# Kernel tuning notes

Measured on AMD Instinct MI355X. Metric: run time of the kernel, lower is better.

Reference implementation:

```python
import jax, jax.numpy as jnp
from jax import lax
import numpy as np

T, B, X, Y = 24, 16, 32, 32
FS, FM, FC = 64, 16, 16
I = FS + FM + FC  # GRU input size = 96
H = 32            # hidden_size


def setup_inputs() -> dict:
    key = jax.random.key(0)
    ks = jax.random.split(key, 8)
    s = 1.0 / np.sqrt(H)  # pytorch GRU init scale
    return {
        "spatial": jax.random.normal(ks[0], (B, X, Y, FS), jnp.float32),
        "meteorology": jax.random.normal(ks[1], (T, B, X, Y, FM), jnp.float32),
        "context": jax.random.normal(ks[2], (T, B, X, Y, FC), jnp.float32),
        "W_ih": jax.random.uniform(ks[3], (3 * H, I), jnp.float32, -s, s),
        "W_hh": jax.random.uniform(ks[4], (3 * H, H), jnp.float32, -s, s),
        "b_ih": jax.random.uniform(ks[5], (3 * H,), jnp.float32, -s, s),
        "b_hh": jax.random.uniform(ks[6], (3 * H,), jnp.float32, -s, s),
        "W": jax.random.normal(ks[7], (H, FS), jnp.float32),
    }


def _gru_final_state(x, W_ih, W_hh, b_ih, b_hh):
    # x: (T, N, I); returns final hidden state (N, H). PyTorch GRU cell math.
    n_batch = x.shape[1]
    h0 = jnp.zeros((n_batch, H), x.dtype)

    def step(h, xt):
        gi = xt @ W_ih.T + b_ih          # (N, 3H)
        gh = h @ W_hh.T + b_hh           # (N, 3H)
        i_r, i_z, i_n = jnp.split(gi, 3, axis=-1)
        h_r, h_z, h_n = jnp.split(gh, 3, axis=-1)
        r = jax.nn.sigmoid(i_r + h_r)
        z = jax.nn.sigmoid(i_z + h_z)
        n = jnp.tanh(i_n + r * h_n)
        h_new = (1.0 - z) * n + z * h
        return h_new, None

    hT, _ = lax.scan(step, h0, x)
    return hT


def reference(spatial, meteorology, context, W_ih, W_hh, b_ih, b_hh, W):
    # Broadcast static spatial features over time and concat along feature dim.
    t = meteorology.shape[0]
    sp = jnp.broadcast_to(spatial[None], (t,) + spatial.shape)
    x = jnp.concatenate([sp, meteorology, context], axis=-1)  # (T,B,X,Y,I)
    # Batch all spatial positions into one recurrence: (T, B*X*Y, I)
    x = x.reshape(t, B * X * Y, I)
    hT = _gru_final_state(x, W_ih, W_hh, b_ih, b_hh)          # (B*X*Y, H)
    out = hT @ W                                              # (B*X*Y, FS)
    return out.reshape(B, X, Y, FS)
```

## Files before the change

kernel.cpp:

```cpp
#include <hip/hip_runtime.h>
#include <hip/hip_fp16.h>
#include <math.h>


typedef __attribute__((ext_vector_type(8))) short short8;
typedef __attribute__((ext_vector_type(8))) _Float16 half8;
typedef __attribute__((ext_vector_type(4))) float f32x4;
typedef __attribute__((ext_vector_type(4))) unsigned int uix4;

#define NSEQ 16384
#define TSTEPS 24
#define LOG2E 1.44269504088896340736f

__device__ __forceinline__ float exp2_fast(float x) {
#if __has_builtin(__builtin_amdgcn_exp2f)
  return __builtin_amdgcn_exp2f(x);
#else
  return __expf(x * 0.6931471805599453f);
#endif
}

__device__ __forceinline__ unsigned int pk_f16(float a, float b) {
#if __has_builtin(__builtin_amdgcn_cvt_pkrtz)
  auto r = __builtin_amdgcn_cvt_pkrtz(a, b);
  return __builtin_bit_cast(unsigned int, r);
#else
  return (unsigned)__half_as_ushort(__float2half(a)) |
         ((unsigned)__half_as_ushort(__float2half(b)) << 16);
#endif
}

__device__ __forceinline__ unsigned int pk_f16_rn(float a, float b) {
  return (unsigned)__half_as_ushort(__float2half(a)) |
         ((unsigned)__half_as_ushort(__float2half(b)) << 16);
}

__device__ __forceinline__ half8 mk_h8(unsigned int a, unsigned int b,
                                       unsigned int c, unsigned int d) {
  uix4 v = {a, b, c, d};
  return __builtin_bit_cast(half8, v);
}

__device__ __forceinline__ f32x4 mfma_h(half8 a, half8 b, f32x4 c) {
  return __builtin_amdgcn_mfma_f32_16x16x32_f16(a, b, c, 0, 0, 0);
}

__device__ __forceinline__ void barrier_lds() {
  asm volatile("s_waitcnt lgkmcnt(0)" ::: "memory");
  __builtin_amdgcn_s_barrier();
}

__global__ __launch_bounds__(256, 4)
void gru8(const float* __restrict__ spatial,
          const float* __restrict__ met,
          const float* __restrict__ ctx,
          const float* __restrict__ W_ih,
          const float* __restrict__ W_hh,
          const float* __restrict__ b_ih,
          const float* __restrict__ b_hh,
          const float* __restrict__ Wp,
          float* __restrict__ out) {
  __shared__ float xls[2][6][16][20];
  __shared__ unsigned int hbuf[2][2][64][2];

  const int tid = threadIdx.x;
  const int lane = tid & 63;
  const int wv = tid >> 6;
  const int l15 = lane & 15;
  const int c = lane >> 4;
  const int seq = blockIdx.x * 16 + l15;
  const f32x4 zero4 = {0.f, 0.f, 0.f, 0.f};

  ((unsigned int*)hbuf[1])[tid] = 0u;

  if (wv >= 2) {
    const int q = wv - 2;
    half8 wmc[3];
    f32x4 acc_i[3];
#pragma unroll
    for (int g = 0; g < 3; ++g) {
      const float sc = (g < 2) ? LOG2E : (2.0f * LOG2E);
      const int rowb = g * 32 + q * 16;
      const float* wrow = W_ih + (size_t)(rowb + l15) * 96 + 64 + c * 8;
      float4 wa = *(const float4*)wrow;
      float4 wb = *(const float4*)(wrow + 4);
      wmc[g] = mk_h8(pk_f16_rn(wa.x * sc, wa.y * sc),
                     pk_f16_rn(wa.z * sc, wa.w * sc),
                     pk_f16_rn(wb.x * sc, wb.y * sc),
                     pk_f16_rn(wb.z * sc, wb.w * sc));
      float4 vih = *(const float4*)(b_ih + rowb + 4 * c);
      if (g < 2) {
        float4 vhh = *(const float4*)(b_hh + rowb + 4 * c);
        acc_i[g][0] = (vih.x + vhh.x) * sc; acc_i[g][1] = (vih.y + vhh.y) * sc;
        acc_i[g][2] = (vih.z + vhh.z) * sc; acc_i[g][3] = (vih.w + vhh.w) * sc;
      } else {
        acc_i[g][0] = vih.x * sc; acc_i[g][1] = vih.y * sc;
        acc_i[g][2] = vih.z * sc; acc_i[g][3] = vih.w * sc;
      }
    }
#pragma unroll
    for (int kt = 0; kt < 2; ++kt) {
      const float* sp = spatial + (size_t)seq * 64 + kt * 32 + c * 8;
      float4 a0 = *(const float4*)sp;
      float4 a1 = *(const float4*)(sp + 4);
      half8 sf = mk_h8(pk_f16(a0.x, a0.y), pk_f16(a0.z, a0.w),
                       pk_f16(a1.x, a1.y), pk_f16(a1.z, a1.w));
#pragma unroll
      for (int g = 0; g < 3; ++g) {
        const float sc = (g < 2) ? LOG2E : (2.0f * LOG2E);
        const float* wrow = W_ih + (size_t)(g * 32 + q * 16 + l15) * 96 +
                            kt * 32 + c * 8;
        float4 wa = *(const float4*)wrow;
        float4 wb = *(const float4*)(wrow + 4);
        half8 wsp = mk_h8(pk_f16_rn(wa.x * sc, wa.y * sc),
                          pk_f16_rn(wa.z * sc, wa.w * sc),
                          pk_f16_rn(wb.x * sc, wb.y * sc),
                          pk_f16_rn(wb.z * sc, wb.w * sc));
        acc_i[g] = mfma_h(wsp, sf, acc_i[g]);
      }
    }
    const float* lptr = ((c < 2) ? met : ctx) + (size_t)seq * 16 + (c & 1) * 8;
    {
      float4 a0 = *(const float4*)lptr;
      float4 a1 = *(const float4*)(lptr + 4);
      half8 xf = mk_h8(pk_f16(a0.x, a0.y), pk_f16(a0.z, a0.w),
                       pk_f16(a1.x, a1.y), pk_f16(a1.z, a1.w));
#pragma unroll
      for (int g = 0; g < 3; ++g) {
        f32x4 D = mfma_h(wmc[g], xf, acc_i[g]);
        *(f32x4*)&xls[0][g * 2 + q][l15][c * 4] = D;
      }
    }
    float4 xs0a = *(const float4*)(lptr + (size_t)1 * NSEQ * 16);
    float4 xs0b = *(const float4*)(lptr + (size_t)1 * NSEQ * 16 + 4);
    float4 xs1a = *(const float4*)(lptr + (size_t)2 * NSEQ * 16);
    float4 xs1b = *(const float4*)(lptr + (size_t)2 * NSEQ * 16 + 4);

    barrier_lds();

#pragma unroll 2
    for (int t = 0; t < TSTEPS; ++t) {
      float4 xa = (t & 1) ? xs1a : xs0a;
      float4 xb = (t & 1) ? xs1b : xs0b;
      half8 xf = mk_h8(pk_f16(xa.x, xa.y), pk_f16(xa.z, xa.w),
                       pk_f16(xb.x, xb.y), pk_f16(xb.z, xb.w));
      {
        int tf = (t + 3 < TSTEPS) ? (t + 3) : (TSTEPS - 1);
        float4 na = *(const float4*)(lptr + (size_t)tf * NSEQ * 16);
        float4 nb = *(const float4*)(lptr + (size_t)tf * NSEQ * 16 + 4);
        if (t & 1) { xs1a = na; xs1b = nb; } else { xs0a = na; xs0b = nb; }
      }
      const int buf = (t + 1) & 1;
#pragma unroll
      for (int g = 0; g < 3; ++g) {
        f32x4 D = mfma_h(wmc[g], xf, acc_i[g]);
        *(f32x4*)&xls[buf][g * 2 + q][l15][c * 4] = D;
      }
      barrier_lds();
    }
  } else {
    const int p = wv;
    __builtin_amdgcn_s_setprio(1);
    half8 whh[3];
#pragma unroll
    for (int g = 0; g < 3; ++g) {
      const float sc = (g < 2) ? LOG2E : (2.0f * LOG2E);
      const float* wrow = W_hh + (size_t)(g * 32 + p * 16 + l15) * 32;
      float4 a = *(const float4*)(wrow + 4 * c);
      float4 b = *(const float4*)(wrow + 16 + 4 * c);
      whh[g] = mk_h8(pk_f16_rn(a.x * sc, a.y * sc),
                     pk_f16_rn(a.z * sc, a.w * sc),
                     pk_f16_rn(b.x * sc, b.y * sc),
                     pk_f16_rn(b.z * sc, b.w * sc));
    }
    f32x4 bhn4;
    {
      float4 v = *(const float4*)(b_hh + 64 + p * 16 + 4 * c);
      bhn4[0] = 2.0f * LOG2E * v.x; bhn4[1] = 2.0f * LOG2E * v.y;
      bhn4[2] = 2.0f * LOG2E * v.z; bhn4[3] = 2.0f * LOG2E * v.w;
    }
    float hst[4] = {0.f, 0.f, 0.f, 0.f};
    unsigned int own0 = 0u, own1 = 0u;

    barrier_lds();

#pragma unroll 2
    for (int t = 0; t < TSTEPS; ++t) {
      const unsigned int* hp = &hbuf[(t + 1) & 1][1 - p][lane][0];
      unsigned int phx = hp[0], phy = hp[1];
      f32x4 xr = *(const f32x4*)&xls[t & 1][p][l15][c * 4];
      f32x4 xz = *(const f32x4*)&xls[t & 1][2 + p][l15][c * 4];
      f32x4 ti = *(const f32x4*)&xls[t & 1][4 + p][l15][c * 4];

      half8 fh = p ? mk_h8(phx, phy, own0, own1)
                   : mk_h8(own0, own1, phx, phy);

      f32x4 d0 = mfma_h(whh[0], fh, xr);
      f32x4 d1 = mfma_h(whh[1], fh, xz);
      f32x4 dn = mfma_h(whh[2], fh, bhn4);

      float hv_[4];
#pragma unroll
      for (int qq = 0; qq < 4; ++qq) {
        float R = exp2_fast(-d0[qq]);
        float r = __builtin_amdgcn_rcpf(1.0f + R);
        float E = fminf(exp2_fast(-d1[qq]), 1e30f);
        float Y = fmaf(r, dn[qq], ti[qq]);
        float e = fminf(exp2_fast(-Y), 1e30f);
        float oe = 1.0f + e, oE = 1.0f + E;
        float inv = __builtin_amdgcn_rcpf(oE * oe);
        float num = fmaf(hst[qq], oe, fmaf(-E, e, E));
        float hv = num * inv;
        hst[qq] = hv;
        hv_[qq] = hv;
      }
      own0 = pk_f16(hv_[0], hv_[1]);
      own1 = pk_f16(hv_[2], hv_[3]);
      hbuf[t & 1][p][lane][0] = own0;
      hbuf[t & 1][p][lane][1] = own1;

      barrier_lds();
    }

    half8 fh;
    {
      const unsigned int* hp = &hbuf[1][1 - p][lane][0];
      unsigned int phx = hp[0], phy = hp[1];
      fh = p ? mk_h8(phx, phy, own0, own1)
             : mk_h8(own0, own1, phx, phy);
    }
#pragma unroll
    for (int pt = 0; pt < 2; ++pt) {
      int ftile = pt * 2 + p;
      int frow = ftile * 16 + l15;
      const float* wpb = Wp + frow;
      float v[8];
#pragma unroll
      for (int e = 0; e < 8; ++e) {
        int col = (e < 4) ? (4 * c + e) : (16 + 4 * c + (e - 4));
        v[e] = wpb[(size_t)col * 64];
      }
      unsigned int uh[4], ul[4];
#pragma unroll
      for (int e2 = 0; e2 < 4; ++e2) {
        float va = v[2 * e2], vb = v[2 * e2 + 1];
        __half ha = __float2half(va), hb = __float2half(vb);
        float la = va - __half2float(ha), lb = vb - __half2float(hb);
        uh[e2] = (unsigned)__half_as_ushort(ha) |
                 ((unsigned)__half_as_ushort(hb) << 16);
        ul[e2] = pk_f16_rn(la, lb);
      }
      half8 wph = mk_h8(uh[0], uh[1], uh[2], uh[3]);
      half8 wpl = mk_h8(ul[0], ul[1], ul[2], ul[3]);
      f32x4 o = mfma_h(wph, fh, zero4);
      o = mfma_h(wpl, fh, o);
      float* op = out + (size_t)seq * 64 + ftile * 16 + 4 * c;
      *(float4*)op = make_float4(o[0], o[1], o[2], o[3]);
    }
    __builtin_amdgcn_s_setprio(0);
  }
}

extern "C" void kernel_launch(void* const* d_in, const int* in_sizes, int n_in,
                              void* d_out, int out_size, void* d_ws, size_t ws_size,
                              hipStream_t stream) {
  const float* spatial = (const float*)d_in[0];
  const float* met     = (const float*)d_in[1];
  const float* ctx     = (const float*)d_in[2];
  const float* W_ih    = (const float*)d_in[3];
  const float* W_hh    = (const float*)d_in[4];
  const float* b_ih    = (const float*)d_in[5];
  const float* b_hh    = (const float*)d_in[6];
  const float* Wp      = (const float*)d_in[7];
  float* out = (float*)d_out;

  hipLaunchKernelGGL(gru8, dim3(1024), dim3(256), 0, stream,
                     spatial, met, ctx, W_ih, W_hh, b_ih, b_hh, Wp, out);
}
```

Before: 25.16 us.

## Collapse GRU block to single wavefront, removing per-step barriers and LDS handoff

Replaces the 4-wave producer/consumer block with a single 64-thread wave per 16 sequences. That wave preloads all timesteps of meteorology and context into LDS as fp16, computes all 6 gate tiles itself, and keeps the hidden state in registers. This removes per-timestep barriers and the LDS exchange of hidden halves between waves, and software-pipelines the input projection one step ahead. The cost is fewer waves per block and a longer serial chain per wave with more MFMA work. It also relies on occupancy from many small blocks to hide latency.

```diff
diff --git a/kernel.cpp b/kernel.cpp
--- a/kernel.cpp
+++ b/kernel.cpp
@@ -3,7 +3,6 @@
 #include <math.h>
 
 
-typedef __attribute__((ext_vector_type(8))) short short8;
 typedef __attribute__((ext_vector_type(8))) _Float16 half8;
 typedef __attribute__((ext_vector_type(4))) float f32x4;
 typedef __attribute__((ext_vector_type(4))) unsigned int uix4;
@@ -29,29 +28,21 @@
          ((unsigned)__half_as_ushort(__float2half(b)) << 16);
 #endif
 }
-
 __device__ __forceinline__ unsigned int pk_f16_rn(float a, float b) {
   return (unsigned)__half_as_ushort(__float2half(a)) |
          ((unsigned)__half_as_ushort(__float2half(b)) << 16);
 }
-
 __device__ __forceinline__ half8 mk_h8(unsigned int a, unsigned int b,
                                        unsigned int c, unsigned int d) {
   uix4 v = {a, b, c, d};
   return __builtin_bit_cast(half8, v);
 }
-
 __device__ __forceinline__ f32x4 mfma_h(half8 a, half8 b, f32x4 c) {
   return __builtin_amdgcn_mfma_f32_16x16x32_f16(a, b, c, 0, 0, 0);
 }
 
-__device__ __forceinline__ void barrier_lds() {
-  asm volatile("s_waitcnt lgkmcnt(0)" ::: "memory");
-  __builtin_amdgcn_s_barrier();
-}
-
-__global__ __launch_bounds__(256, 4)
-void gru8(const float* __restrict__ spatial,
+__global__ __launch_bounds__(64, 1)
+void gru9(const float* __restrict__ spatial,
           const float* __restrict__ met,
           const float* __restrict__ ctx,
           const float* __restrict__ W_ih,
@@ -60,204 +51,180 @@
           const float* __restrict__ b_hh,
           const float* __restrict__ Wp,
           float* __restrict__ out) {
-  __shared__ float xls[2][6][16][20];
-  __shared__ unsigned int hbuf[2][2][64][2];
-
-  const int tid = threadIdx.x;
-  const int lane = tid & 63;
-  const int wv = tid >> 6;
+  __shared__ unsigned int xst[TSTEPS][16][16];
+
+  const int lane = threadIdx.x & 63;
   const int l15 = lane & 15;
   const int c = lane >> 4;
   const int seq = blockIdx.x * 16 + l15;
   const f32x4 zero4 = {0.f, 0.f, 0.f, 0.f};
 
-  ((unsigned int*)hbuf[1])[tid] = 0u;
-
-  if (wv >= 2) {
-    const int q = wv - 2;
-    half8 wmc[3];
-    f32x4 acc_i[3];
-#pragma unroll
-    for (int g = 0; g < 3; ++g) {
-      const float sc = (g < 2) ? LOG2E : (2.0f * LOG2E);
-      const int rowb = g * 32 + q * 16;
-      const float* wrow = W_ih + (size_t)(rowb + l15) * 96 + 64 + c * 8;
-      float4 wa = *(const float4*)wrow;
-      float4 wb = *(const float4*)(wrow + 4);
-      wmc[g] = mk_h8(pk_f16_rn(wa.x * sc, wa.y * sc),
-                     pk_f16_rn(wa.z * sc, wa.w * sc),
-                     pk_f16_rn(wb.x * sc, wb.y * sc),
-                     pk_f16_rn(wb.z * sc, wb.w * sc));
-      float4 vih = *(const float4*)(b_ih + rowb + 4 * c);
-      if (g < 2) {
-        float4 vhh = *(const float4*)(b_hh + rowb + 4 * c);
-        acc_i[g][0] = (vih.x + vhh.x) * sc; acc_i[g][1] = (vih.y + vhh.y) * sc;
-        acc_i[g][2] = (vih.z + vhh.z) * sc; acc_i[g][3] = (vih.w + vhh.w) * sc;
-      } else {
-        acc_i[g][0] = vih.x * sc; acc_i[g][1] = vih.y * sc;
-        acc_i[g][2] = vih.z * sc; acc_i[g][3] = vih.w * sc;
-      }
-    }
-#pragma unroll
-    for (int kt = 0; kt < 2; ++kt) {
-      const float* sp = spatial + (size_t)seq * 64 + kt * 32 + c * 8;
-      float4 a0 = *(const float4*)sp;
-      float4 a1 = *(const float4*)(sp + 4);
-      half8 sf = mk_h8(pk_f16(a0.x, a0.y), pk_f16(a0.z, a0.w),
-                       pk_f16(a1.x, a1.y), pk_f16(a1.z, a1.w));
-#pragma unroll
-      for (int g = 0; g < 3; ++g) {
-        const float sc = (g < 2) ? LOG2E : (2.0f * LOG2E);
-        const float* wrow = W_ih + (size_t)(g * 32 + q * 16 + l15) * 96 +
-                            kt * 32 + c * 8;
-        float4 wa = *(const float4*)wrow;
-        float4 wb = *(const float4*)(wrow + 4);
-        half8 wsp = mk_h8(pk_f16_rn(wa.x * sc, wa.y * sc),
-                          pk_f16_rn(wa.z * sc, wa.w * sc),
-                          pk_f16_rn(wb.x * sc, wb.y * sc),
-                          pk_f16_rn(wb.z * sc, wb.w * sc));
-        acc_i[g] = mfma_h(wsp, sf, acc_i[g]);
-      }
-    }
-    const float* lptr = ((c < 2) ? met : ctx) + (size_t)seq * 16 + (c & 1) * 8;
-    {
-      float4 a0 = *(const float4*)lptr;
-      float4 a1 = *(const float4*)(lptr + 4);
-      half8 xf = mk_h8(pk_f16(a0.x, a0.y), pk_f16(a0.z, a0.w),
-                       pk_f16(a1.x, a1.y), pk_f16(a1.z, a1.w));
-#pragma unroll
-      for (int g = 0; g < 3; ++g) {
-        f32x4 D = mfma_h(wmc[g], xf, acc_i[g]);
-        *(f32x4*)&xls[0][g * 2 + q][l15][c * 4] = D;
-      }
-    }
-    float4 xs0a = *(const float4*)(lptr + (size_t)1 * NSEQ * 16);
-    float4 xs0b = *(const float4*)(lptr + (size_t)1 * NSEQ * 16 + 4);
-    float4 xs1a = *(const float4*)(lptr + (size_t)2 * NSEQ * 16);
-    float4 xs1b = *(const float4*)(lptr + (size_t)2 * NSEQ * 16 + 4);
-
-    barrier_lds();
-
-#pragma unroll 2
-    for (int t = 0; t < TSTEPS; ++t) {
-      float4 xa = (t & 1) ? xs1a : xs0a;
-      float4 xb = (t & 1) ? xs1b : xs0b;
-      half8 xf = mk_h8(pk_f16(xa.x, xa.y), pk_f16(xa.z, xa.w),
-                       pk_f16(xb.x, xb.y), pk_f16(xb.z, xb.w));
-      {
-        int tf = (t + 3 < TSTEPS) ? (t + 3) : (TSTEPS - 1);
-        float4 na = *(const float4*)(lptr + (size_t)tf * NSEQ * 16);
-        float4 nb = *(const float4*)(lptr + (size_t)tf * NSEQ * 16 + 4);
-        if (t & 1) { xs1a = na; xs1b = nb; } else { xs0a = na; xs0b = nb; }
-      }
-      const int buf = (t + 1) & 1;
-#pragma unroll
-      for (int g = 0; g < 3; ++g) {
-        f32x4 D = mfma_h(wmc[g], xf, acc_i[g]);
-        *(f32x4*)&xls[buf][g * 2 + q][l15][c * 4] = D;
-      }
-      barrier_lds();
-    }
-  } else {
-    const int p = wv;
-    __builtin_amdgcn_s_setprio(1);
-    half8 whh[3];
-#pragma unroll
-    for (int g = 0; g < 3; ++g) {
-      const float sc = (g < 2) ? LOG2E : (2.0f * LOG2E);
-      const float* wrow = W_hh + (size_t)(g * 32 + p * 16 + l15) * 32;
-      float4 a = *(const float4*)(wrow + 4 * c);
-      float4 b = *(const float4*)(wrow + 16 + 4 * c);
-      whh[g] = mk_h8(pk_f16_rn(a.x * sc, a.y * sc),
-                     pk_f16_rn(a.z * sc, a.w * sc),
-                     pk_f16_rn(b.x * sc, b.y * sc),
-                     pk_f16_rn(b.z * sc, b.w * sc));
-    }
-    f32x4 bhn4;
-    {
-      float4 v = *(const float4*)(b_hh + 64 + p * 16 + 4 * c);
-      bhn4[0] = 2.0f * LOG2E * v.x; bhn4[1] = 2.0f * LOG2E * v.y;
-      bhn4[2] = 2.0f * LOG2E * v.z; bhn4[3] = 2.0f * LOG2E * v.w;
-    }
-    float hst[4] = {0.f, 0.f, 0.f, 0.f};
-    unsigned int own0 = 0u, own1 = 0u;
-
-    barrier_lds();
-
-#pragma unroll 2
-    for (int t = 0; t < TSTEPS; ++t) {
-      const unsigned int* hp = &hbuf[(t + 1) & 1][1 - p][lane][0];
-      unsigned int phx = hp[0], phy = hp[1];
-      f32x4 xr = *(const f32x4*)&xls[t & 1][p][l15][c * 4];
-      f32x4 xz = *(const f32x4*)&xls[t & 1][2 + p][l15][c * 4];
-      f32x4 ti = *(const f32x4*)&xls[t & 1][4 + p][l15][c * 4];
-
-      half8 fh = p ? mk_h8(phx, phy, own0, own1)
-                   : mk_h8(own0, own1, phx, phy);
-
-      f32x4 d0 = mfma_h(whh[0], fh, xr);
-      f32x4 d1 = mfma_h(whh[1], fh, xz);
-      f32x4 dn = mfma_h(whh[2], fh, bhn4);
-
-      float hv_[4];
-#pragma unroll
-      for (int qq = 0; qq < 4; ++qq) {
-        float R = exp2_fast(-d0[qq]);
+#pragma unroll
+  for (int tt = 0; tt < 6; ++tt) {
+    const int t = c + tt * 4;
+    const float* mp = met + ((size_t)t * NSEQ + seq) * 16;
+    const float* cp = ctx + ((size_t)t * NSEQ + seq) * 16;
+    float4 m0 = *(const float4*)mp;       float4 m1 = *(const float4*)(mp + 4);
+    float4 m2 = *(const float4*)(mp + 8); float4 m3 = *(const float4*)(mp + 12);
+    float4 c0 = *(const float4*)cp;       float4 c1 = *(const float4*)(cp + 4);
+    float4 c2 = *(const float4*)(cp + 8); float4 c3 = *(const float4*)(cp + 12);
+    unsigned int* dst = &xst[t][l15][0];
+    uix4 w0 = {pk_f16(m0.x, m0.y), pk_f16(m0.z, m0.w),
+               pk_f16(m1.x, m1.y), pk_f16(m1.z, m1.w)};
+    uix4 w1 = {pk_f16(m2.x, m2.y), pk_f16(m2.z, m2.w),
+               pk_f16(m3.x, m3.y), pk_f16(m3.z, m3.w)};
+    uix4 w2 = {pk_f16(c0.x, c0.y), pk_f16(c0.z, c0.w),
+               pk_f16(c1.x, c1.y), pk_f16(c1.z, c1.w)};
+    uix4 w3 = {pk_f16(c2.x, c2.y), pk_f16(c2.z, c2.w),
+               pk_f16(c3.x, c3.y), pk_f16(c3.z, c3.w)};
+    *(uix4*)&dst[0]  = w0;  *(uix4*)&dst[4]  = w1;
+    *(uix4*)&dst[8]  = w2;  *(uix4*)&dst[12] = w3;
+  }
+
+  half8 whh[6], wmc[6];
+  f32x4 acc_i[6], bhnA, bhnB;
+#pragma unroll
+  for (int j = 0; j < 6; ++j) {
+    const float sc = (j < 4) ? LOG2E : (2.0f * LOG2E);
+    const float* wr = W_hh + (size_t)(j * 16 + l15) * 32;
+    float4 a = *(const float4*)(wr + 4 * c);
+    float4 b = *(const float4*)(wr + 16 + 4 * c);
+    whh[j] = mk_h8(pk_f16_rn(a.x * sc, a.y * sc), pk_f16_rn(a.z * sc, a.w * sc),
+                   pk_f16_rn(b.x * sc, b.y * sc), pk_f16_rn(b.z * sc, b.w * sc));
+    const float* mr = W_ih + (size_t)(j * 16 + l15) * 96 + 64 + c * 8;
+    float4 wa = *(const float4*)mr;
+    float4 wb = *(const float4*)(mr + 4);
+    wmc[j] = mk_h8(pk_f16_rn(wa.x * sc, wa.y * sc), pk_f16_rn(wa.z * sc, wa.w * sc),
+                   pk_f16_rn(wb.x * sc, wb.y * sc), pk_f16_rn(wb.z * sc, wb.w * sc));
+    const int rowb = j * 16 + 4 * c;
+    float4 vih = *(const float4*)(b_ih + rowb);
+    if (j < 4) {
+      float4 vhh = *(const float4*)(b_hh + rowb);
+      acc_i[j][0] = (vih.x + vhh.x) * sc; acc_i[j][1] = (vih.y + vhh.y) * sc;
+      acc_i[j][2] = (vih.z + vhh.z) * sc; acc_i[j][3] = (vih.w + vhh.w) * sc;
+    } else {
+      acc_i[j][0] = vih.x * sc; acc_i[j][1] = vih.y * sc;
+      acc_i[j][2] = vih.z * sc; acc_i[j][3] = vih.w * sc;
+    }
+  }
+  {
+    float4 va = *(const float4*)(b_hh + 64 + 4 * c);
+    float4 vb = *(const float4*)(b_hh + 64 + 16 + 4 * c);
+    bhnA[0] = 2.0f * LOG2E * va.x; bhnA[1] = 2.0f * LOG2E * va.y;
+    bhnA[2] = 2.0f * LOG2E * va.z; bhnA[3] = 2.0f * LOG2E * va.w;
+    bhnB[0] = 2.0f * LOG2E * vb.x; bhnB[1] = 2.0f * LOG2E * vb.y;
+    bhnB[2] = 2.0f * LOG2E * vb.z; bhnB[3] = 2.0f * LOG2E * vb.w;
+  }
+
+#pragma unroll
+  for (int kt = 0; kt < 2; ++kt) {
+    const float* sp = spatial + (size_t)seq * 64 + kt * 32 + c * 8;
+    float4 a0 = *(const float4*)sp;
+    float4 a1 = *(const float4*)(sp + 4);
+    half8 sf = mk_h8(pk_f16(a0.x, a0.y), pk_f16(a0.z, a0.w),
+                     pk_f16(a1.x, a1.y), pk_f16(a1.z, a1.w));
+#pragma unroll
+    for (int j = 0; j < 6; ++j) {
+      const float sc = (j < 4) ? LOG2E : (2.0f * LOG2E);
+      const float* wr = W_ih + (size_t)(j * 16 + l15) * 96 + kt * 32 + c * 8;
+      float4 wa = *(const float4*)wr;
+      float4 wb = *(const float4*)(wr + 4);
+      half8 wsp = mk_h8(pk_f16_rn(wa.x * sc, wa.y * sc),
+                        pk_f16_rn(wa.z * sc, wa.w * sc),
+                        pk_f16_rn(wb.x * sc, wb.y * sc),
+                        pk_f16_rn(wb.z * sc, wb.w * sc));
+      acc_i[j] = mfma_h(wsp, sf, acc_i[j]);
+    }
+  }
+
+  f32x4 xacc[6];
+  {
+    uix4 v = *(const uix4*)&xst[0][l15][c * 4];
+    half8 xf = __builtin_bit_cast(half8, v);
+#pragma unroll
+    for (int j = 0; j < 6; ++j) xacc[j] = mfma_h(wmc[j], xf, acc_i[j]);
+  }
+  half8 xf1;
+  {
+    uix4 v = *(const uix4*)&xst[1][l15][c * 4];
+    xf1 = __builtin_bit_cast(half8, v);
+  }
+
+  float hst[8];
+#pragma unroll
+  for (int i = 0; i < 8; ++i) hst[i] = 0.0f;
+  half8 fh = mk_h8(0u, 0u, 0u, 0u);
+
+#pragma unroll 4
+  for (int t = 0; t < TSTEPS; ++t) {
+    f32x4 dr0 = mfma_h(whh[0], fh, xacc[0]);
+    f32x4 dr1 = mfma_h(whh[1], fh, xacc[1]);
+    f32x4 dz0 = mfma_h(whh[2], fh, xacc[2]);
+    f32x4 dz1 = mfma_h(whh[3], fh, xacc[3]);
+    f32x4 th0 = mfma_h(whh[4], fh, bhnA);
+    f32x4 th1 = mfma_h(whh[5], fh, bhnB);
+    f32x4 ti0 = xacc[4], ti1 = xacc[5];
+
+#pragma unroll
+    for (int j = 0; j < 6; ++j) xacc[j] = mfma_h(wmc[j], xf1, acc_i[j]);
+    if (t + 2 < TSTEPS) {
+      uix4 v = *(const uix4*)&xst[t + 2][l15][c * 4];
+      xf1 = __builtin_bit_cast(half8, v);
+    }
+
+    float hv_[8];
+#pragma unroll
+    for (int jj = 0; jj < 2; ++jj) {
+      f32x4 ddr = jj ? dr1 : dr0;
+      f32x4 ddz = jj ? dz1 : dz0;
+      f32x4 tth = jj ? th1 : th0;
+      f32x4 tti = jj ? ti1 : ti0;
+#pragma unroll
+      for (int q = 0; q < 4; ++q) {
+        const int i = jj * 4 + q;
+        float R = exp2_fast(-ddr[q]);
         float r = __builtin_amdgcn_rcpf(1.0f + R);
-        float E = fminf(exp2_fast(-d1[qq]), 1e30f);
-        float Y = fmaf(r, dn[qq], ti[qq]);
+        float E = fminf(exp2_fast(-ddz[q]), 1e30f);
+        float Y = fmaf(r, tth[q], tti[q]);
         float e = fminf(exp2_fast(-Y), 1e30f);
         float oe = 1.0f + e, oE = 1.0f + E;
         float inv = __builtin_amdgcn_rcpf(oE * oe);
-        float num = fmaf(hst[qq], oe, fmaf(-E, e, E));
+        float num = fmaf(hst[i], oe, fmaf(-E, e, E));
         float hv = num * inv;
-        hst[qq] = hv;
-        hv_[qq] = hv;
+        hst[i] = hv;
+        hv_[i] = hv;
       }
-      own0 = pk_f16(hv_[0], hv_[1]);
-      own1 = pk_f16(hv_[2], hv_[3]);
-      hbuf[t & 1][p][lane][0] = own0;
-      hbuf[t & 1][p][lane][1] = own1;
-
-      barrier_lds();
-    }
-
-    half8 fh;
-    {
-      const unsigned int* hp = &hbuf[1][1 - p][lane][0];
-      unsigned int phx = hp[0], phy = hp[1];
-      fh = p ? mk_h8(phx, phy, own0, own1)
-             : mk_h8(own0, own1, phx, phy);
-    }
-#pragma unroll
-    for (int pt = 0; pt < 2; ++pt) {
-      int ftile = pt * 2 + p;
-      int frow = ftile * 16 + l15;
-      const float* wpb = Wp + frow;
-      float v[8];
-#pragma unroll
-      for (int e = 0; e < 8; ++e) {
-        int col = (e < 4) ? (4 * c + e) : (16 + 4 * c + (e - 4));
-        v[e] = wpb[(size_t)col * 64];
-      }
-      unsigned int uh[4], ul[4];
-#pragma unroll
-      for (int e2 = 0; e2 < 4; ++e2) {
-        float va = v[2 * e2], vb = v[2 * e2 + 1];
-        __half ha = __float2half(va), hb = __float2half(vb);
-        float la = va - __half2float(ha), lb = vb - __half2float(hb);
-        uh[e2] = (unsigned)__half_as_ushort(ha) |
-                 ((unsigned)__half_as_ushort(hb) << 16);
-        ul[e2] = pk_f16_rn(la, lb);
-      }
-      half8 wph = mk_h8(uh[0], uh[1], uh[2], uh[3]);
-      half8 wpl = mk_h8(ul[0], ul[1], ul[2], ul[3]);
-      f32x4 o = mfma_h(wph, fh, zero4);
-      o = mfma_h(wpl, fh, o);
-      float* op = out + (size_t)seq * 64 + ftile * 16 + 4 * c;
-      *(float4*)op = make_float4(o[0], o[1], o[2], o[3]);
-    }
-    __builtin_amdgcn_s_setprio(0);
+    }
+    fh = mk_h8(pk_f16(hv_[0], hv_[1]), pk_f16(hv_[2], hv_[3]),
+               pk_f16(hv_[4], hv_[5]), pk_f16(hv_[6], hv_[7]));
+  }
+
+#pragma unroll
+  for (int pt = 0; pt < 4; ++pt) {
+    const int frow = pt * 16 + l15;
+    const float* wpb = Wp + frow;
+    float v[8];
+#pragma unroll
+    for (int e = 0; e < 8; ++e) {
+      int col = (e < 4) ? (4 * c + e) : (16 + 4 * c + (e - 4));
+      v[e] = wpb[(size_t)col * 64];
+    }
+    unsigned int uh[4], ul[4];
+#pragma unroll
+    for (int e2 = 0; e2 < 4; ++e2) {
+      float va = v[2 * e2], vb = v[2 * e2 + 1];
+      __half ha = __float2half(va), hb = __float2half(vb);
+      float la = va - __half2float(ha), lb = vb - __half2float(hb);
+      uh[e2] = (unsigned)__half_as_ushort(ha) |
+               ((unsigned)__half_as_ushort(hb) << 16);
+      ul[e2] = pk_f16_rn(la, lb);
+    }
+    half8 wph = mk_h8(uh[0], uh[1], uh[2], uh[3]);
+    half8 wpl = mk_h8(ul[0], ul[1], ul[2], ul[3]);
+    f32x4 o = mfma_h(wph, fh, zero4);
+    o = mfma_h(wpl, fh, o);
+    float* op = out + (size_t)seq * 64 + pt * 16 + 4 * c;
+    *(float4*)op = make_float4(o[0], o[1], o[2], o[3]);
   }
 }
 
@@ -274,6 +241,6 @@
   const float* Wp      = (const float*)d_in[7];
   float* out = (float*)d_out;
 
-  hipLaunchKernelGGL(gru8, dim3(1024), dim3(256), 0, stream,
+  hipLaunchKernelGGL(gru9, dim3(1024), dim3(64), 0, stream,
                      spatial, met, ctx, W_ih, W_hh, b_ih, b_hh, Wp, out);
 }
```

After: 30.38 us. +20.8%, slower.
